# Kernel optimization log

Hardware: AMD Instinct MI355X
Metric: run time of the kernel (lower is better)

Reference implementation:

```python
import jax, jax.numpy as jnp
import numpy as np

N = 100000    # nodes ('paper')
E = 600000    # edges per relation
R = 3         # relations (etypes)
IN = 256      # in_feats
HF = 256      # h_feats
H = 4         # n_heads
D = HF // H   # per-head dim
C = 153       # num_classes
NEG_SLOPE = 0.2


def setup_inputs() -> dict:
    key = jax.random.key(0)
    ks = jax.random.split(key, 14)
    s = 0.05
    x = jax.random.normal(ks[0], (N, IN), jnp.float32)
    src = jax.random.randint(ks[1], (R, E), 0, N, jnp.int32)
    dst = jax.random.randint(ks[2], (R, E), 0, N, jnp.int32)
    # layer 1 params (per relation): fc weight, attn_l, attn_r, bias
    W1 = jax.random.normal(ks[3], (R, IN, HF), jnp.float32) * s
    al1 = jax.random.normal(ks[4], (R, H, D), jnp.float32) * s
    ar1 = jax.random.normal(ks[5], (R, H, D), jnp.float32) * s
    b1 = jax.random.normal(ks[6], (R, HF), jnp.float32) * s
    # layer 2 params
    W2 = jax.random.normal(ks[7], (R, HF, HF), jnp.float32) * s
    al2 = jax.random.normal(ks[8], (R, H, D), jnp.float32) * s
    ar2 = jax.random.normal(ks[9], (R, H, D), jnp.float32) * s
    b2 = jax.random.normal(ks[10], (R, HF), jnp.float32) * s
    # output linear
    Wout = jax.random.normal(ks[11], (HF, C), jnp.float32) * s
    bout = jax.random.normal(ks[12], (C,), jnp.float32) * s
    return {"x": x, "src": src, "dst": dst,
            "W1": W1, "al1": al1, "ar1": ar1, "b1": b1,
            "W2": W2, "al2": al2, "ar2": ar2, "b2": b2,
            "Wout": Wout, "bout": bout}


def _hetero_gat_layer(h, src, dst, W, al, ar, b):
    """HeteroGraphConv over R relations of GATConv, aggregate='sum'.
    h: [N, F_in] -> returns [N, H, D]."""
    acc = jnp.zeros((N, H, D), h.dtype)
    for r in range(R):  # small fixed relation set
        sr, dr = src[r], dst[r]
        feat = (h @ W[r]).reshape(N, H, D)           # projected [N,H,D]
        el = jnp.sum(feat * al[r], axis=-1)          # [N,H]
        er = jnp.sum(feat * ar[r], axis=-1)          # [N,H]
        e = jax.nn.leaky_relu(el[sr] + er[dr], NEG_SLOPE)  # [E,H]
        # edge softmax per destination node, per head
        m = jax.ops.segment_max(e, dr, num_segments=N)     # [N,H]
        a = jnp.exp(e - m[dr])                             # [E,H]
        z = jax.ops.segment_sum(a, dr, num_segments=N)     # [N,H]
        alpha = a / z[dr]                                  # [E,H]
        msg = feat[sr] * alpha[:, :, None]                 # [E,H,D]
        out = jax.ops.segment_sum(msg, dr, num_segments=N) # [N,H,D]
        acc = acc + out + b[r].reshape(1, H, D)
    return acc


def reference(x, src, dst, W1, al1, ar1, b1, W2, al2, ar2, b2, Wout, bout):
    h = _hetero_gat_layer(x, src, dst, W1, al1, ar1, b1).reshape(N, HF)
    h = jax.nn.relu(h)  # apply_each(h, F.relu); dropout is identity in eval
    h = _hetero_gat_layer(h, src, dst, W2, al2, ar2, b2).reshape(N, HF)
    return h @ Wout + bout  # self.linear(h['paper'])
```

## Files before the change

kernel.cpp:

```cpp
#include <hip/hip_runtime.h>
#include <hip/hip_bf16.h>

#define NN 100000
#define EE 600000
#define RR 3
#define INF 256
#define HFF 256
#define NH 4
#define DD 64
#define CC 153
#define NB 98

typedef __attribute__((ext_vector_type(8))) _Float16 f16x8;
typedef __attribute__((ext_vector_type(2))) _Float16 h2f16;
typedef __attribute__((ext_vector_type(4))) float f32x4;
typedef __attribute__((ext_vector_type(2))) unsigned int u32x2;

#define GLDS(g, l) __builtin_amdgcn_global_load_lds((const __attribute__((address_space(1))) void*)(g), \
                                                    (__attribute__((address_space(3))) void*)(l), 16, 0, 0)

static __device__ __forceinline__ unsigned short f2h(float x) {
    _Float16 h = (_Float16)x;
    return __builtin_bit_cast(unsigned short, h);
}
static __device__ __forceinline__ float h2f(unsigned short u) {
    return (float)__builtin_bit_cast(_Float16, u);
}

template<int GM>
__global__ __launch_bounds__(256) void mfma_gemm(const unsigned short* __restrict__ A,
                                                 const unsigned short* __restrict__ Bt,
                                                 const float* __restrict__ bias,
                                                 float* __restrict__ C32,
                                                 unsigned short* __restrict__ C16,
                                                 const float* __restrict__ al,
                                                 const float* __restrict__ ar,
                                                 float* __restrict__ el,
                                                 float* __restrict__ er,
                                                 int M) {
    __shared__ __align__(1024) char lds[32768];
    const int tid = threadIdx.x;
    const int lane = tid & 63;
    const int w = tid >> 6;
    const int wr = w >> 1, wc = w & 1;
    const int bm = blockIdx.x * 128;
    const int bn = blockIdx.y * 128;

    f32x4 acc[4][4] = {};

    const int lrow8 = lane >> 3;
    const int cbs = ((lane & 7) << 4) ^ ((lrow8 & 7) << 4);
    const int cbase = w * 8;
    const bool isA = (w < 2);

    const char* gA = (const char*)A;
    const char* gB = (const char*)Bt;

    for (int step = 0; step < 4; ++step) {
        const int k0b = step * 128;
#pragma unroll
        for (int i = 0; i < 8; ++i) {
            int c = cbase + i;
            char* lptr = &lds[c * 1024];
            if (isA) {
                int R = c * 8 + lrow8;
                int grow = bm + R; if (grow >= M) grow = M - 1;
                GLDS(gA + (size_t)grow * 512 + k0b + cbs, lptr);
            } else {
                int nIdx = (c - 16) * 8 + lrow8;
                GLDS(gB + (size_t)(bn + nIdx) * 512 + k0b + cbs, lptr);
            }
        }
        __syncthreads();
#pragma unroll
        for (int kk = 0; kk < 2; ++kk) {
            f16x8 af[4], bfr[4];
            const int o = kk * 64 + ((lane >> 4) << 4);
#pragma unroll
            for (int m = 0; m < 4; ++m) {
                int R = wr * 64 + m * 16 + (lane & 15);
                af[m] = *reinterpret_cast<const f16x8*>(&lds[R * 128 + (o ^ ((R & 7) << 4))]);
            }
#pragma unroll
            for (int n = 0; n < 4; ++n) {
                int Rn = wc * 64 + n * 16 + (lane & 15);
                bfr[n] = *reinterpret_cast<const f16x8*>(&lds[16384 + Rn * 128 + (o ^ ((Rn & 7) << 4))]);
            }
#pragma unroll
            for (int m = 0; m < 4; ++m)
#pragma unroll
                for (int n = 0; n < 4; ++n)
                    acc[m][n] = __builtin_amdgcn_mfma_f32_16x16x32_f16(af[m], bfr[n], acc[m][n], 0, 0, 0);
        }
        __syncthreads();
    }

    const int rb = bm + wr * 64 + ((lane >> 4) << 2);

    if (GM == 0) {
        const int cb2 = bn + wc * 64 + (lane & 15);
#pragma unroll
        for (int m = 0; m < 4; ++m)
#pragma unroll
            for (int n = 0; n < 4; ++n) {
                int col = cb2 + n * 16;
                if (col < CC) {
                    float bb = bias[col];
#pragma unroll
                    for (int j = 0; j < 4; ++j) {
                        int row = rb + m * 16 + j;
                        if (row < M) C32[(size_t)row * CC + col] = acc[m][n][j] + bb;
                    }
                }
            }
    } else {
        const int c0 = bn + wc * 64;
        const int rh = c0 >> 6;
        const int rw = rh >> 2;
        const int h  = rh & 3;
        float alv[4], arv[4];
#pragma unroll
        for (int n = 0; n < 4; ++n) {
            alv[n] = al[rh * 64 + n * 16 + (lane & 15)];
            arv[n] = ar[rh * 64 + n * 16 + (lane & 15)];
        }
#pragma unroll
        for (int m = 0; m < 4; ++m)
#pragma unroll
            for (int j = 0; j < 4; ++j) {
                float pl = acc[m][0][j] * alv[0] + acc[m][1][j] * alv[1]
                         + acc[m][2][j] * alv[2] + acc[m][3][j] * alv[3];
                float pr = acc[m][0][j] * arv[0] + acc[m][1][j] * arv[1]
                         + acc[m][2][j] * arv[2] + acc[m][3][j] * arv[3];
#pragma unroll
                for (int o2 = 1; o2 < 16; o2 <<= 1) {
                    pl += __shfl_xor(pl, o2);
                    pr += __shfl_xor(pr, o2);
                }
                int row = rb + m * 16 + j;
                if ((lane & 15) == 0 && row < M) {
                    el[(size_t)rw * NN * 4 + row * 4 + h] = pl;
                    er[(size_t)rw * NN * 4 + row * 4 + h] = pr;
                }
            }
        __syncthreads();
        unsigned short* l16 = (unsigned short*)lds;
#pragma unroll
        for (int m = 0; m < 4; ++m)
#pragma unroll
            for (int n = 0; n < 4; ++n)
#pragma unroll
                for (int j = 0; j < 4; ++j) {
                    int row = wr * 64 + m * 16 + ((lane >> 4) << 2) + j;
                    int colb = (wc * 64 + n * 16 + (lane & 15)) * 2;
                    int addr = row * 256 + (colb ^ (((row >> 2) & 7) << 5));
                    l16[addr >> 1] = f2h(acc[m][n][j]);
                }
        __syncthreads();
        const int rblk = bn >> 8;
        const int bnc  = bn & 255;
        const size_t NFE = (size_t)NN * 256;
#pragma unroll
        for (int i = 0; i < 8; ++i) {
            int seg = w * 8 + i;
            int row = seg * 4 + (lane >> 4);
            int colb = (lane & 15) * 16;
            int addr = row * 256 + (colb ^ (((row >> 2) & 7) << 5));
            uint4 v = *reinterpret_cast<const uint4*>(&lds[addr]);
            int grow = bm + row;
            if (grow < M) {
                unsigned short* gp = C16 + (size_t)rblk * NFE + (size_t)grow * 256 + bnc + (lane & 15) * 8;
                *reinterpret_cast<uint4*>(gp) = v;
            }
        }
    }
}

__global__ __launch_bounds__(256) void f2h4(const float* __restrict__ in,
                                            unsigned short* __restrict__ out, int n4) {
    int i = blockIdx.x * 256 + threadIdx.x;
    if (i >= n4) return;
    float4 v = reinterpret_cast<const float4*>(in)[i];
    ushort4 o;
    o.x = f2h(v.x); o.y = f2h(v.y); o.z = f2h(v.z); o.w = f2h(v.w);
    reinterpret_cast<ushort4*>(out)[i] = o;
}

__global__ __launch_bounds__(256) void wprep_kernel(const float* __restrict__ W1,
                                                    const float* __restrict__ W2,
                                                    const float* __restrict__ Wout,
                                                    unsigned short* __restrict__ Wt,
                                                    unsigned short* __restrict__ Woutt) {
    int idx = blockIdx.x * 256 + threadIdx.x;
    const int NW = 2 * RR * 65536;
    if (idx < NW) {
        int lyr = idx >= RR * 65536;
        int rem2 = idx - lyr * RR * 65536;
        int r = rem2 >> 16, rem = rem2 & 65535;
        int n = rem >> 8, k = rem & 255;
        const float* W = lyr ? W2 : W1;
        Wt[idx] = f2h(W[(r << 16) + (k << 8) + n]);
    } else if (idx < NW + 65536) {
        int rem = idx - NW;
        int n = rem >> 8, k = rem & 255;
        Woutt[rem] = (n < CC) ? f2h(Wout[k * CC + n]) : (unsigned short)0;
    }
}

__global__ __launch_bounds__(256) void hist_kernel(const int* __restrict__ dst,
                                                   int* __restrict__ deg) {
    int i = blockIdx.x * 256 + threadIdx.x;
    if (i >= RR * EE) return;
    int r = i / EE;
    atomicAdd(&deg[r * NN + dst[i]], 1);
}

__global__ __launch_bounds__(256) void scan_block(const int* __restrict__ deg,
                                                  int* __restrict__ rowptr,
                                                  int* __restrict__ bsum) {
    __shared__ int sh[256];
    int r = blockIdx.y, b = blockIdx.x, t = threadIdx.x;
    int base = b * 1024;
    int v[4];
#pragma unroll
    for (int j = 0; j < 4; ++j) {
        int idx = base + t * 4 + j;
        v[j] = (idx < NN) ? deg[r * NN + idx] : 0;
    }
    int tsum = v[0] + v[1] + v[2] + v[3];
    sh[t] = tsum;
    __syncthreads();
    for (int off = 1; off < 256; off <<= 1) {
        int x = (t >= off) ? sh[t - off] : 0;
        __syncthreads();
        sh[t] += x;
        __syncthreads();
    }
    int run = sh[t] - tsum;
#pragma unroll
    for (int j = 0; j < 4; ++j) {
        int idx = base + t * 4 + j;
        if (idx < NN) rowptr[r * (NN + 1) + idx] = run;
        run += v[j];
    }
    if (t == 255) bsum[r * NB + b] = run;
}

__global__ void scan_bsum(int* __restrict__ bsum, int* __restrict__ rowptr) {
    int r = threadIdx.x;
    if (r >= RR) return;
    int run = 0;
    for (int b = 0; b < NB; ++b) {
        int x = bsum[r * NB + b];
        bsum[r * NB + b] = run;
        run += x;
    }
    rowptr[r * (NN + 1) + NN] = run;
}

__global__ __launch_bounds__(256) void add_off(int* __restrict__ rowptr,
                                               const int* __restrict__ bsum) {
    int r = blockIdx.y, b = blockIdx.x, t = threadIdx.x;
    int o = bsum[r * NB + b];
#pragma unroll
    for (int j = 0; j < 4; ++j) {
        int idx = b * 1024 + t * 4 + j;
        if (idx < NN) rowptr[r * (NN + 1) + idx] += o;
    }
}

__global__ __launch_bounds__(256) void fill_kernel(const int* __restrict__ src,
                                                   const int* __restrict__ dst,
                                                   const int* __restrict__ rowptr,
                                                   int* __restrict__ cursor,
                                                   int* __restrict__ csrc) {
    int i = blockIdx.x * 256 + threadIdx.x;
    if (i >= RR * EE) return;
    int r = i / EE;
    int d = dst[i], s = src[i];
    int pos = rowptr[r * (NN + 1) + d] + atomicAdd(&cursor[r * NN + d], 1);
    csrc[(size_t)r * EE + pos] = s;
}

template<int RELU>
__global__ __launch_bounds__(256) void agg3_kernel(const int* __restrict__ csrc,
                                                   const int* __restrict__ rowptr,
                                                   const float* __restrict__ el,
                                                   const float* __restrict__ er,
                                                   const unsigned short* __restrict__ feat,
                                                   const float* __restrict__ brel,
                                                   unsigned short* __restrict__ hout) {
    int wid = (blockIdx.x * 256 + threadIdx.x) >> 6;
    int lane = threadIdx.x & 63;
    if (wid >= NN) return;
    int d = wid;
    int h = lane >> 4;
    int f0 = lane * 4;

    float4 bA = *reinterpret_cast<const float4*>(brel + f0);
    float4 bB = *reinterpret_cast<const float4*>(brel + 256 + f0);
    float4 bC = *reinterpret_cast<const float4*>(brel + 512 + f0);
    float4 cur = make_float4(bA.x + bB.x + bC.x, bA.y + bB.y + bC.y,
                             bA.z + bB.z + bC.z, bA.w + bB.w + bC.w);

#pragma unroll
    for (int r = 0; r < RR; ++r) {
        int p0 = rowptr[r * (NN + 1) + d], p1 = rowptr[r * (NN + 1) + d + 1];
        if (p0 == p1) continue;
        float erd = er[(size_t)r * NN * 4 + d * 4 + h];
        const float* elr = el + (size_t)r * NN * 4;
        const unsigned short* fr = feat + (size_t)r * NN * 256;
        const int* cs = csrc + (size_t)r * EE;

        h2f16 aA01 = (h2f16)0, aA23 = (h2f16)0;
        h2f16 aB01 = (h2f16)0, aB23 = (h2f16)0;
        float zs = 0.f;
        int last = p1 - 1;
        for (int p = p0; p < p1; p += 4) {
            int q1 = p + 1 <= last ? p + 1 : last;
            int q2 = p + 2 <= last ? p + 2 : last;
            int q3 = p + 3 <= last ? p + 3 : last;
            int s0 = __builtin_nontemporal_load(cs + p);
            int s1 = __builtin_nontemporal_load(cs + q1);
            int s2 = __builtin_nontemporal_load(cs + q2);
            int s3 = __builtin_nontemporal_load(cs + q3);
            uint2 fA = *reinterpret_cast<const uint2*>(fr + (size_t)s0 * 256 + f0);
            uint2 fB = *reinterpret_cast<const uint2*>(fr + (size_t)s1 * 256 + f0);
            uint2 fC = *reinterpret_cast<const uint2*>(fr + (size_t)s2 * 256 + f0);
            uint2 fD = *reinterpret_cast<const uint2*>(fr + (size_t)s3 * 256 + f0);
            float v0 = elr[s0 * 4 + h] + erd;
            float v1 = elr[s1 * 4 + h] + erd;
            float v2 = elr[s2 * 4 + h] + erd;
            float v3 = elr[s3 * 4 + h] + erd;
            v0 = v0 > 0.f ? v0 : 0.2f * v0;
            v1 = v1 > 0.f ? v1 : 0.2f * v1;
            v2 = v2 > 0.f ? v2 : 0.2f * v2;
            v3 = v3 > 0.f ? v3 : 0.2f * v3;
            float w0 = __expf(v0);
            float w1 = (p + 1 <= last) ? __expf(v1) : 0.f;
            float w2 = (p + 2 <= last) ? __expf(v2) : 0.f;
            float w3 = (p + 3 <= last) ? __expf(v3) : 0.f;
            zs += (w0 + w1) + (w2 + w3);
            _Float16 h0 = (_Float16)w0, h1 = (_Float16)w1;
            _Float16 h2 = (_Float16)w2, h3 = (_Float16)w3;
            h2f16 wp0 = (h2f16){h0, h0}, wp1 = (h2f16){h1, h1};
            h2f16 wp2 = (h2f16){h2, h2}, wp3 = (h2f16){h3, h3};
            aA01 += wp0 * __builtin_bit_cast(h2f16, fA.x);
            aA23 += wp0 * __builtin_bit_cast(h2f16, fA.y);
            aB01 += wp1 * __builtin_bit_cast(h2f16, fB.x);
            aB23 += wp1 * __builtin_bit_cast(h2f16, fB.y);
            aA01 += wp2 * __builtin_bit_cast(h2f16, fC.x);
            aA23 += wp2 * __builtin_bit_cast(h2f16, fC.y);
            aB01 += wp3 * __builtin_bit_cast(h2f16, fD.x);
            aB23 += wp3 * __builtin_bit_cast(h2f16, fD.y);
        }
        float inv = 1.f / zs;
        cur.x += ((float)aA01[0] + (float)aB01[0]) * inv;
        cur.y += ((float)aA01[1] + (float)aB01[1]) * inv;
        cur.z += ((float)aA23[0] + (float)aB23[0]) * inv;
        cur.w += ((float)aA23[1] + (float)aB23[1]) * inv;
    }
    if (RELU) {
        cur.x = fmaxf(cur.x, 0.f); cur.y = fmaxf(cur.y, 0.f);
        cur.z = fmaxf(cur.z, 0.f); cur.w = fmaxf(cur.w, 0.f);
    }
    ushort4 o;
    o.x = f2h(cur.x); o.y = f2h(cur.y); o.z = f2h(cur.z); o.w = f2h(cur.w);
    u32x2 ov = __builtin_bit_cast(u32x2, o);
    __builtin_nontemporal_store(ov, reinterpret_cast<u32x2*>(hout + (size_t)d * 256 + f0));
}

extern "C" void kernel_launch(void* const* d_in, const int* in_sizes, int n_in,
                              void* d_out, int out_size, void* d_ws, size_t ws_size,
                              hipStream_t stream) {
    const float* x    = (const float*)d_in[0];
    const int*   src  = (const int*)d_in[1];
    const int*   dst  = (const int*)d_in[2];
    const float* W1   = (const float*)d_in[3];
    const float* al1  = (const float*)d_in[4];
    const float* ar1  = (const float*)d_in[5];
    const float* b1   = (const float*)d_in[6];
    const float* W2   = (const float*)d_in[7];
    const float* al2  = (const float*)d_in[8];
    const float* ar2  = (const float*)d_in[9];
    const float* b2   = (const float*)d_in[10];
    const float* Wout = (const float*)d_in[11];
    const float* bout = (const float*)d_in[12];
    float* out = (float*)d_out;

    char* base = (char*)d_ws;
    size_t off = 0;
    auto alloc = [&](size_t bytes) -> char* {
        char* p = base + off;
        off = (off + bytes + 255) & ~(size_t)255;
        return p;
    };
    size_t NF = (size_t)NN * HFF;
    unsigned short* feath = (unsigned short*)alloc(RR * NF * 2);
    float* el   = (float*)alloc((size_t)RR * NN * NH * 4);
    float* er   = (float*)alloc((size_t)RR * NN * NH * 4);
    int* deg    = (int*)alloc((size_t)RR * NN * 4 * 2);
    int* cursor = deg + (size_t)RR * NN;
    int* rowptr = (int*)alloc((size_t)RR * (NN + 1) * 4);
    int* bsum   = (int*)alloc((size_t)RR * NB * 4);
    int* csrc   = (int*)alloc((size_t)RR * EE * 4);
    unsigned short* xh    = (unsigned short*)alloc(NF * 2);
    unsigned short* wth   = (unsigned short*)alloc((size_t)2 * RR * 65536 * 2);
    unsigned short* wouth = (unsigned short*)alloc((size_t)65536 * 2);

    int n4Blocks = (int)((NF / 4 + 255) / 256);
    int reBlocks = (RR * EE + 255) / 256;
    int aggBlocks = (NN * 64 + 255) / 256;
    dim3 pgrid((NN + 127) / 128, 6);
    dim3 ogrid((NN + 127) / 128, 2);
    int wpBlocks = (2 * RR * 65536 + 65536) / 256;

    hipMemsetAsync(deg, 0, (size_t)RR * NN * sizeof(int) * 2, stream);
    hist_kernel<<<reBlocks, 256, 0, stream>>>(dst, deg);
    scan_block<<<dim3(NB, RR), 256, 0, stream>>>(deg, rowptr, bsum);
    scan_bsum<<<1, 64, 0, stream>>>(bsum, rowptr);
    add_off<<<dim3(NB, RR), 256, 0, stream>>>(rowptr, bsum);
    fill_kernel<<<reBlocks, 256, 0, stream>>>(src, dst, rowptr, cursor, csrc);

    f2h4<<<n4Blocks, 256, 0, stream>>>(x, xh, (int)(NF / 4));
    wprep_kernel<<<wpBlocks, 256, 0, stream>>>(W1, W2, Wout, wth, wouth);

    for (int layer = 0; layer < 2; ++layer) {
        const float* al = layer ? al2 : al1;
        const float* ar = layer ? ar2 : ar1;
        const float* b  = layer ? b2 : b1;
        const unsigned short* wl = wth + (size_t)layer * RR * 65536;

        mfma_gemm<1><<<pgrid, 256, 0, stream>>>(xh, wl, nullptr,
                                                nullptr, feath, al, ar, el, er, NN);
        if (layer == 0)
            agg3_kernel<1><<<aggBlocks, 256, 0, stream>>>(csrc, rowptr, el, er, feath, b, xh);
        else
            agg3_kernel<0><<<aggBlocks, 256, 0, stream>>>(csrc, rowptr, el, er, feath, b, xh);
    }

    mfma_gemm<0><<<ogrid, 256, 0, stream>>>(xh, wouth, bout, out, nullptr,
                                            nullptr, nullptr, nullptr, nullptr, NN);
}
```

Measured before the change: 831.6 us.

## Split each node's edge aggregation across two wavefronts with LDS reduction

The aggregation kernel now assigns two wavefronts per destination node, each processing half of the incoming edges for every relation. Partial feature sums and softmax denominators are written to shared memory and combined by one wave after a barrier. This doubles the memory-level parallelism per node to hide gather latency, at the cost of twice the waves, LDS traffic, and a block-wide sync. Nontemporal loads and stores are also swapped for regular accesses.

```diff
diff --git a/kernel.cpp b/kernel.cpp
--- a/kernel.cpp
+++ b/kernel.cpp
@@ -14,7 +14,6 @@
 typedef __attribute__((ext_vector_type(8))) _Float16 f16x8;
 typedef __attribute__((ext_vector_type(2))) _Float16 h2f16;
 typedef __attribute__((ext_vector_type(4))) float f32x4;
-typedef __attribute__((ext_vector_type(2))) unsigned int u32x2;
 
 #define GLDS(g, l) __builtin_amdgcn_global_load_lds((const __attribute__((address_space(1))) void*)(g), \
                                                     (__attribute__((address_space(3))) void*)(l), 16, 0, 0)
@@ -290,75 +289,98 @@
                                                    const unsigned short* __restrict__ feat,
                                                    const float* __restrict__ brel,
                                                    unsigned short* __restrict__ hout) {
-    int wid = (blockIdx.x * 256 + threadIdx.x) >> 6;
-    int lane = threadIdx.x & 63;
-    if (wid >= NN) return;
-    int d = wid;
-    int h = lane >> 4;
-    int f0 = lane * 4;
+    __shared__ float4 lacc[2][2][RR][64];
+    __shared__ float  lz[2][2][RR][NH];
+    const int tid = threadIdx.x;
+    const int wv = tid >> 6;
+    const int lane = tid & 63;
+    const int dw = wv >> 1, half = wv & 1;
+    const int d = blockIdx.x * 2 + dw;
+    const bool valid = d < NN;
+    const int h = lane >> 4;
+    const int f0 = lane * 4;
+
+#pragma unroll
+    for (int r = 0; r < RR; ++r) {
+        h2f16 aA01 = (h2f16)0, aA23 = (h2f16)0;
+        h2f16 aB01 = (h2f16)0, aB23 = (h2f16)0;
+        float zs = 0.f;
+        if (valid) {
+            int p0 = rowptr[r * (NN + 1) + d], p1 = rowptr[r * (NN + 1) + d + 1];
+            int mid = (p0 + p1 + 1) >> 1;
+            int q0 = half ? mid : p0;
+            int q1 = half ? p1 : mid;
+            if (q0 < q1) {
+                float erd = er[(size_t)r * NN * 4 + d * 4 + h];
+                const float* elr = el + (size_t)r * NN * 4;
+                const unsigned short* fr = feat + (size_t)r * NN * 256;
+                const int* cs = csrc + (size_t)r * EE;
+                int last = q1 - 1;
+                for (int p = q0; p < q1; p += 4) {
+                    int e1 = p + 1 <= last ? p + 1 : last;
+                    int e2 = p + 2 <= last ? p + 2 : last;
+                    int e3 = p + 3 <= last ? p + 3 : last;
+                    int s0 = cs[p], s1 = cs[e1], s2 = cs[e2], s3 = cs[e3];
+                    uint2 fA = *reinterpret_cast<const uint2*>(fr + (size_t)s0 * 256 + f0);
+                    uint2 fB = *reinterpret_cast<const uint2*>(fr + (size_t)s1 * 256 + f0);
+                    uint2 fC = *reinterpret_cast<const uint2*>(fr + (size_t)s2 * 256 + f0);
+                    uint2 fD = *reinterpret_cast<const uint2*>(fr + (size_t)s3 * 256 + f0);
+                    float v0 = elr[s0 * 4 + h] + erd;
+                    float v1 = elr[s1 * 4 + h] + erd;
+                    float v2 = elr[s2 * 4 + h] + erd;
+                    float v3 = elr[s3 * 4 + h] + erd;
+                    v0 = v0 > 0.f ? v0 : 0.2f * v0;
+                    v1 = v1 > 0.f ? v1 : 0.2f * v1;
+                    v2 = v2 > 0.f ? v2 : 0.2f * v2;
+                    v3 = v3 > 0.f ? v3 : 0.2f * v3;
+                    float w0 = __expf(v0);
+                    float w1 = (p + 1 <= last) ? __expf(v1) : 0.f;
+                    float w2 = (p + 2 <= last) ? __expf(v2) : 0.f;
+                    float w3 = (p + 3 <= last) ? __expf(v3) : 0.f;
+                    zs += (w0 + w1) + (w2 + w3);
+                    _Float16 h0 = (_Float16)w0, h1 = (_Float16)w1;
+                    _Float16 h2 = (_Float16)w2, h3 = (_Float16)w3;
+                    h2f16 wp0 = (h2f16){h0, h0}, wp1 = (h2f16){h1, h1};
+                    h2f16 wp2 = (h2f16){h2, h2}, wp3 = (h2f16){h3, h3};
+                    aA01 += wp0 * __builtin_bit_cast(h2f16, fA.x);
+                    aA23 += wp0 * __builtin_bit_cast(h2f16, fA.y);
+                    aB01 += wp1 * __builtin_bit_cast(h2f16, fB.x);
+                    aB23 += wp1 * __builtin_bit_cast(h2f16, fB.y);
+                    aA01 += wp2 * __builtin_bit_cast(h2f16, fC.x);
+                    aA23 += wp2 * __builtin_bit_cast(h2f16, fC.y);
+                    aB01 += wp3 * __builtin_bit_cast(h2f16, fD.x);
+                    aB23 += wp3 * __builtin_bit_cast(h2f16, fD.y);
+                }
+            }
+        }
+        float4 part;
+        part.x = (float)aA01[0] + (float)aB01[0];
+        part.y = (float)aA01[1] + (float)aB01[1];
+        part.z = (float)aA23[0] + (float)aB23[0];
+        part.w = (float)aA23[1] + (float)aB23[1];
+        lacc[dw][half][r][lane] = part;
+        if ((lane & 15) == 0) lz[dw][half][r][h] = zs;
+    }
+    __syncthreads();
+    if (half || !valid) return;
 
     float4 bA = *reinterpret_cast<const float4*>(brel + f0);
     float4 bB = *reinterpret_cast<const float4*>(brel + 256 + f0);
     float4 bC = *reinterpret_cast<const float4*>(brel + 512 + f0);
     float4 cur = make_float4(bA.x + bB.x + bC.x, bA.y + bB.y + bC.y,
                              bA.z + bB.z + bC.z, bA.w + bB.w + bC.w);
-
 #pragma unroll
     for (int r = 0; r < RR; ++r) {
-        int p0 = rowptr[r * (NN + 1) + d], p1 = rowptr[r * (NN + 1) + d + 1];
-        if (p0 == p1) continue;
-        float erd = er[(size_t)r * NN * 4 + d * 4 + h];
-        const float* elr = el + (size_t)r * NN * 4;
-        const unsigned short* fr = feat + (size_t)r * NN * 256;
-        const int* cs = csrc + (size_t)r * EE;
-
-        h2f16 aA01 = (h2f16)0, aA23 = (h2f16)0;
-        h2f16 aB01 = (h2f16)0, aB23 = (h2f16)0;
-        float zs = 0.f;
-        int last = p1 - 1;
-        for (int p = p0; p < p1; p += 4) {
-            int q1 = p + 1 <= last ? p + 1 : last;
-            int q2 = p + 2 <= last ? p + 2 : last;
-            int q3 = p + 3 <= last ? p + 3 : last;
-            int s0 = __builtin_nontemporal_load(cs + p);
-            int s1 = __builtin_nontemporal_load(cs + q1);
-            int s2 = __builtin_nontemporal_load(cs + q2);
-            int s3 = __builtin_nontemporal_load(cs + q3);
-            uint2 fA = *reinterpret_cast<const uint2*>(fr + (size_t)s0 * 256 + f0);
-            uint2 fB = *reinterpret_cast<const uint2*>(fr + (size_t)s1 * 256 + f0);
-            uint2 fC = *reinterpret_cast<const uint2*>(fr + (size_t)s2 * 256 + f0);
-            uint2 fD = *reinterpret_cast<const uint2*>(fr + (size_t)s3 * 256 + f0);
-            float v0 = elr[s0 * 4 + h] + erd;
-            float v1 = elr[s1 * 4 + h] + erd;
-            float v2 = elr[s2 * 4 + h] + erd;
-            float v3 = elr[s3 * 4 + h] + erd;
-            v0 = v0 > 0.f ? v0 : 0.2f * v0;
-            v1 = v1 > 0.f ? v1 : 0.2f * v1;
-            v2 = v2 > 0.f ? v2 : 0.2f * v2;
-            v3 = v3 > 0.f ? v3 : 0.2f * v3;
-            float w0 = __expf(v0);
-            float w1 = (p + 1 <= last) ? __expf(v1) : 0.f;
-            float w2 = (p + 2 <= last) ? __expf(v2) : 0.f;
-            float w3 = (p + 3 <= last) ? __expf(v3) : 0.f;
-            zs += (w0 + w1) + (w2 + w3);
-            _Float16 h0 = (_Float16)w0, h1 = (_Float16)w1;
-            _Float16 h2 = (_Float16)w2, h3 = (_Float16)w3;
-            h2f16 wp0 = (h2f16){h0, h0}, wp1 = (h2f16){h1, h1};
-            h2f16 wp2 = (h2f16){h2, h2}, wp3 = (h2f16){h3, h3};
-            aA01 += wp0 * __builtin_bit_cast(h2f16, fA.x);
-            aA23 += wp0 * __builtin_bit_cast(h2f16, fA.y);
-            aB01 += wp1 * __builtin_bit_cast(h2f16, fB.x);
-            aB23 += wp1 * __builtin_bit_cast(h2f16, fB.y);
-            aA01 += wp2 * __builtin_bit_cast(h2f16, fC.x);
-            aA23 += wp2 * __builtin_bit_cast(h2f16, fC.y);
-            aB01 += wp3 * __builtin_bit_cast(h2f16, fD.x);
-            aB23 += wp3 * __builtin_bit_cast(h2f16, fD.y);
-        }
-        float inv = 1.f / zs;
-        cur.x += ((float)aA01[0] + (float)aB01[0]) * inv;
-        cur.y += ((float)aA01[1] + (float)aB01[1]) * inv;
-        cur.z += ((float)aA23[0] + (float)aB23[0]) * inv;
-        cur.w += ((float)aA23[1] + (float)aB23[1]) * inv;
+        float z = lz[dw][0][r][h] + lz[dw][1][r][h];
+        if (z > 0.f) {
+            float4 a0 = lacc[dw][0][r][lane];
+            float4 a1 = lacc[dw][1][r][lane];
+            float inv = 1.f / z;
+            cur.x += (a0.x + a1.x) * inv;
+            cur.y += (a0.y + a1.y) * inv;
+            cur.z += (a0.z + a1.z) * inv;
+            cur.w += (a0.w + a1.w) * inv;
+        }
     }
     if (RELU) {
         cur.x = fmaxf(cur.x, 0.f); cur.y = fmaxf(cur.y, 0.f);
@@ -366,8 +388,7 @@
     }
     ushort4 o;
     o.x = f2h(cur.x); o.y = f2h(cur.y); o.z = f2h(cur.z); o.w = f2h(cur.w);
-    u32x2 ov = __builtin_bit_cast(u32x2, o);
-    __builtin_nontemporal_store(ov, reinterpret_cast<u32x2*>(hout + (size_t)d * 256 + f0));
+    *reinterpret_cast<ushort4*>(hout + (size_t)d * 256 + f0) = o;
 }
 
 extern "C" void kernel_launch(void* const* d_in, const int* in_sizes, int n_in,
@@ -410,7 +431,7 @@
 
     int n4Blocks = (int)((NF / 4 + 255) / 256);
     int reBlocks = (RR * EE + 255) / 256;
-    int aggBlocks = (NN * 64 + 255) / 256;
+    int aggBlocks = (NN + 1) / 2;
     dim3 pgrid((NN + 127) / 128, 6);
     dim3 ogrid((NN + 127) / 128, 2);
     int wpBlocks = (2 * RR * 65536 + 65536) / 256;
```

Measured after the change: 839.4 us. Within noise of the previous version (+0.9%).
